# Kernel optimization log

Measured on AMD Instinct MI355X. Metric: run time of the kernel, lower is better.

The kernel has to match this reference:

```python
import jax, jax.numpy as jnp
import numpy as np

HEADS = 4
DIM_HEAD = 32


def setup_inputs() -> dict:
    key = jax.random.key(0)
    k1, k2, k3 = jax.random.split(key, 3)
    B, L, D = 16, 8192, 256
    hidden = HEADS * DIM_HEAD  # 128
    x = jax.random.normal(k1, (B, L, D), dtype=jnp.float32)
    W_qkv = jax.random.normal(k2, (D, 3 * hidden), dtype=jnp.float32) * (D ** -0.5)
    W_out = jax.random.normal(k3, (hidden, D), dtype=jnp.float32) * (hidden ** -0.5)
    b_out = jnp.zeros((D,), dtype=jnp.float32)
    return {"x": x, "W_qkv": W_qkv, "W_out": W_out, "b_out": b_out}


def reference(x, W_qkv, W_out, b_out):
    B, L, D = x.shape
    scale = DIM_HEAD ** -0.5
    # 1x1 conv == per-token matmul
    qkv = jnp.einsum('bld,df->blf', x, W_qkv)  # [B, L, 3*h*dh]
    qkv = qkv.reshape(B, L, 3, HEADS, DIM_HEAD)
    q = jnp.transpose(qkv[:, :, 0], (0, 2, 1, 3)) * scale          # [B, h, L, d]
    k = jax.nn.softmax(jnp.transpose(qkv[:, :, 1], (0, 2, 1, 3)), axis=2)  # softmax over L
    v = jnp.transpose(qkv[:, :, 2], (0, 2, 1, 3))                  # [B, h, L, e]
    context = jnp.einsum('bhld,bhle->bhde', k, v)                  # [B, h, d, e]
    out = jnp.einsum('bhde,bhld->bhle', context, q)                # [B, h, L, e]
    out = jnp.transpose(out, (0, 2, 1, 3)).reshape(B, L, HEADS * DIM_HEAD)
    return jnp.einsum('blf,fd->bld', out, W_out) + b_out
```

## Files before the change

kernel.cpp:

```cpp
#include <hip/hip_runtime.h>
#include <math.h>


#define BL 131072

typedef __attribute__((ext_vector_type(8))) short bf16x8;
typedef __attribute__((ext_vector_type(4))) float f32x4;
typedef __attribute__((ext_vector_type(4))) unsigned u32x4;

__device__ __forceinline__ unsigned cvt_pk2(float a, float b) {
    unsigned r;
    asm("v_cvt_pk_bf16_f32 %0, %1, %2" : "=v"(r) : "v"(a), "v"(b));
    return r;
}
__device__ __forceinline__ ushort bf16_rn(float f) {
    return (ushort)cvt_pk2(f, f);
}
__device__ __forceinline__ float bf16f(ushort h) { return __uint_as_float(((unsigned)h) << 16); }

__device__ __forceinline__ void glds16(const void* g, void* l) {
    __builtin_amdgcn_global_load_lds((const __attribute__((address_space(1))) unsigned int*)g,
                                     (__attribute__((address_space(3))) unsigned int*)l,
                                     16, 0, 0);
}

__global__ __launch_bounds__(256) void prep_kernel(const float* __restrict__ W,
                                                   ushort* __restrict__ wh,
                                                   ushort* __restrict__ wl,
                                                   float* __restrict__ S,
                                                   float* __restrict__ Z) {
    int n = blockIdx.x, k = threadIdx.x;
    float f = W[k * 384 + n];
    ushort h = bf16_rn(f);
    wh[n * 256 + k] = h;
    wl[n * 256 + k] = bf16_rn(f - bf16f(h));
    int i = n * 256 + k;
    if (i < 65536) S[i] = 0.f;
    if (i < 2048) Z[i] = 0.f;
}

__global__ __launch_bounds__(256) void gemm1_kernel(
    const float* __restrict__ X,
    const ushort* __restrict__ Wh, const ushort* __restrict__ Wl,
    ushort* __restrict__ Qh, ushort* __restrict__ Ql,
    float* __restrict__ KV) {
    __shared__ __align__(16) float  As[2][4096];
    __shared__ __align__(16) ushort Bsh[2][4096];
    __shared__ __align__(16) ushort Bsl[2][4096];
    const int tid = threadIdx.x;
    const int wg = blockIdx.x;
    const int xcd = wg & 7;
    const int slot = wg >> 3;
    const int cb = slot % 3;
    const int yb = (slot / 3) * 8 + xcd;
    const int col0 = cb * 128;
    const int row0 = yb * 128;
    const int lane = tid & 63, wave = tid >> 6;
    const int wr = (wave & 1) * 64, wc = (wave >> 1) * 64;
    const int m = lane & 15, quad = lane >> 4;
    const int ra = lane >> 3, pa = lane & 7;
    const int rb = lane >> 2, pb = lane & 3;

    f32x4 acc[4][4] = {};

    auto STAGE = [&](int buf, int k0) {
#pragma unroll
        for (int s = 0; s < 4; ++s) {
            int seg = s * 4 + wave;
            int r = seg * 8 + ra;
            int q = pa ^ (r & 7);
            glds16(&X[(long)(row0 + r) * 256 + k0 + q * 4], &As[buf][seg * 256]);
        }
#pragma unroll
        for (int s = 0; s < 2; ++s) {
            int seg = s * 4 + wave;
            int r = seg * 16 + rb;
            int q = pb ^ ((r >> 1) & 3);
            glds16(&Wh[(long)(col0 + r) * 256 + k0 + q * 8], &Bsh[buf][seg * 512]);
            glds16(&Wl[(long)(col0 + r) * 256 + k0 + q * 8], &Bsl[buf][seg * 512]);
        }
    };

    STAGE(0, 0);
    __syncthreads();

    for (int kt = 0; kt < 8; ++kt) {
        const int cur = kt & 1;
        if (kt < 7) STAGE(cur ^ 1, (kt + 1) * 32);

        bf16x8 bh[4], bl[4];
#pragma unroll
        for (int i = 0; i < 4; ++i) {
            int r = wc + i * 16 + m;
            int p = quad ^ ((r >> 1) & 3);
            bh[i] = *(const bf16x8*)&Bsh[cur][r * 32 + p * 8];
            bl[i] = *(const bf16x8*)&Bsl[cur][r * 32 + p * 8];
        }
#pragma unroll
        for (int i = 0; i < 4; ++i) {
            int r = wr + i * 16 + m;
            int p0 = (quad * 2) ^ (r & 7);
            int p1 = (quad * 2 + 1) ^ (r & 7);
            f32x4 a0 = *(const f32x4*)&As[cur][r * 32 + p0 * 4];
            f32x4 a1 = *(const f32x4*)&As[cur][r * 32 + p1 * 4];
            u32x4 ahw, alw;
#pragma unroll
            for (int e = 0; e < 2; ++e) {
                float f0 = a0[2 * e], f1 = a0[2 * e + 1];
                unsigned h = cvt_pk2(f0, f1);
                ahw[e] = h;
                alw[e] = cvt_pk2(f0 - __uint_as_float(h << 16),
                                 f1 - __uint_as_float(h & 0xFFFF0000u));
            }
#pragma unroll
            for (int e = 0; e < 2; ++e) {
                float f0 = a1[2 * e], f1 = a1[2 * e + 1];
                unsigned h = cvt_pk2(f0, f1);
                ahw[2 + e] = h;
                alw[2 + e] = cvt_pk2(f0 - __uint_as_float(h << 16),
                                     f1 - __uint_as_float(h & 0xFFFF0000u));
            }
            bf16x8 ah = __builtin_bit_cast(bf16x8, ahw);
            bf16x8 al = __builtin_bit_cast(bf16x8, alw);
#pragma unroll
            for (int j = 0; j < 4; ++j) {
                acc[i][j] = __builtin_amdgcn_mfma_f32_16x16x32_bf16(ah, bh[j], acc[i][j], 0, 0, 0);
                acc[i][j] = __builtin_amdgcn_mfma_f32_16x16x32_bf16(ah, bl[j], acc[i][j], 0, 0, 0);
                acc[i][j] = __builtin_amdgcn_mfma_f32_16x16x32_bf16(al, bh[j], acc[i][j], 0, 0, 0);
            }
        }
        __syncthreads();
    }

    if (cb == 0) {
#pragma unroll
        for (int i = 0; i < 4; ++i)
#pragma unroll
            for (int r4 = 0; r4 < 4; ++r4) {
                long row = row0 + wr + i * 16 + quad * 4 + r4;
#pragma unroll
                for (int j = 0; j < 4; ++j) {
                    float v = acc[i][j][r4];
                    int col = wc + j * 16 + m;
                    ushort h = bf16_rn(v);
                    Qh[row * 128 + col] = h;
                    Ql[row * 128 + col] = bf16_rn(v - bf16f(h));
                }
            }
    } else {
        int vofs = (cb == 2) ? 32 : 0;
#pragma unroll
        for (int i = 0; i < 4; ++i)
#pragma unroll
            for (int r4 = 0; r4 < 4; ++r4) {
                long row = row0 + wr + i * 16 + quad * 4 + r4;
                long b = row >> 13, l = row & 8191;
#pragma unroll
                for (int j = 0; j < 4; ++j) {
                    int c = wc + j * 16 + m;
                    int h = c >> 5, dd = c & 31;
                    KV[(((b * 4 + h) * 8192 + l) * 64) + vofs + dd] = acc[i][j][r4];
                }
            }
    }
}

__global__ __launch_bounds__(256) void ksum_hb(const float* __restrict__ KV,
                                               float* __restrict__ S,
                                               float* __restrict__ Z) {
    int bx = blockIdx.x;
    int chunk = bx & 7, bh = bx >> 3;
    const float* slab = KV + ((long)bh * 8192 + chunk * 1024) * 64;
    __shared__ float tile[4128];
    const int tid = threadIdx.x;
    const int w = tid >> 6, lane = tid & 63;
    const int lg = lane >> 3, cc = lane & 7;
    const int combo = w * 8 + cc;
    const int d0 = (combo >> 2) * 4;
    const int e0 = (combo & 3) * 8;
    const int c4 = tid & 15, lrow = tid >> 4;
    float z4[4] = {0.f, 0.f, 0.f, 0.f};
    float acc[4][8] = {};

    for (int t0 = 0; t0 < 1024; t0 += 64) {
#pragma unroll
        for (int u = 0; u < 4; ++u) {
            int l = u * 16 + lrow;
            float4 wv = *(const float4*)&slab[((long)(t0 + l)) * 64 + c4 * 4];
            if (c4 < 8) { wv.x = __expf(wv.x); wv.y = __expf(wv.y); wv.z = __expf(wv.z); wv.w = __expf(wv.w); }
            *(float4*)&tile[l * 64 + (l >> 3) * 4 + c4 * 4] = wv;
        }
        __syncthreads();
#pragma unroll
        for (int j = 0; j < 8; ++j) {
            int l = lg * 8 + j;
            int base = l * 64 + lg * 4;
            f32x4 ev = *(const f32x4*)&tile[base + d0];
            f32x4 v0 = *(const f32x4*)&tile[base + 32 + e0];
            f32x4 v1 = *(const f32x4*)&tile[base + 36 + e0];
#pragma unroll
            for (int q = 0; q < 4; ++q) {
                float e = ev[q];
                z4[q] += e;
                acc[q][0] += e * v0[0]; acc[q][1] += e * v0[1];
                acc[q][2] += e * v0[2]; acc[q][3] += e * v0[3];
                acc[q][4] += e * v1[0]; acc[q][5] += e * v1[1];
                acc[q][6] += e * v1[2]; acc[q][7] += e * v1[3];
            }
        }
        __syncthreads();
    }
#pragma unroll
    for (int q = 0; q < 4; ++q) {
        z4[q] += __shfl_xor(z4[q], 8);
        z4[q] += __shfl_xor(z4[q], 16);
        z4[q] += __shfl_xor(z4[q], 32);
#pragma unroll
        for (int j = 0; j < 8; ++j) {
            acc[q][j] += __shfl_xor(acc[q][j], 8);
            acc[q][j] += __shfl_xor(acc[q][j], 16);
            acc[q][j] += __shfl_xor(acc[q][j], 32);
        }
    }
    if (lg == 0) {
#pragma unroll
        for (int q = 0; q < 4; ++q)
#pragma unroll
            for (int j = 0; j < 8; ++j)
                atomicAdd(&S[((long)bh * 32 + d0 + q) * 32 + e0 + j], acc[q][j]);
        if ((cc & 3) == 0)
#pragma unroll
            for (int q = 0; q < 4; ++q)
                atomicAdd(&Z[bh * 32 + d0 + q], z4[q]);
    }
}

__global__ __launch_bounds__(256) void combine_kernel(const float* __restrict__ S,
                                                      const float* __restrict__ Z,
                                                      const float* __restrict__ Wout,
                                                      ushort* __restrict__ m2h,
                                                      ushort* __restrict__ m2l) {
    int bh = blockIdx.x;
    int b = bh >> 2, h = bh & 3;
    int n = threadIdx.x;
    __shared__ float ctx[32][32];
    __shared__ float zs[32];
    if (n < 32) zs[n] = Z[bh * 32 + n];
    __syncthreads();
#pragma unroll
    for (int t = 0; t < 4; ++t) {
        int idx = t * 256 + n;
        int d = idx >> 5, e = idx & 31;
        ctx[d][e] = S[(long)bh * 1024 + idx] / zs[d];
    }
    __syncthreads();
    const float scale = 0.17677669529663687f;
    float acc[32];
#pragma unroll
    for (int d = 0; d < 32; ++d) acc[d] = 0.f;
    for (int e = 0; e < 32; ++e) {
        float w = Wout[(h * 32 + e) * 256 + n];
#pragma unroll
        for (int d = 0; d < 32; ++d) acc[d] += ctx[d][e] * w;
    }
#pragma unroll
    for (int d = 0; d < 32; ++d) {
        float v = acc[d] * scale;
        long idx = ((long)(b * 256 + n)) * 128 + h * 32 + d;
        ushort hh = bf16_rn(v);
        m2h[idx] = hh;
        m2l[idx] = bf16_rn(v - bf16f(hh));
    }
}

__global__ __launch_bounds__(256) void gemm2_kernel(
    const ushort* __restrict__ Ahp, const ushort* __restrict__ Alp,
    const ushort* __restrict__ Bhp, const ushort* __restrict__ Blp,
    const float* __restrict__ bias, float* __restrict__ out) {
    __shared__ __align__(16) ushort Ash[2][4096];
    __shared__ __align__(16) ushort Asl[2][4096];
    __shared__ __align__(16) ushort Bsh[2][4096];
    __shared__ __align__(16) ushort Bsl[2][4096];
    const int tid = threadIdx.x;
    const int bid = blockIdx.x;
    const int xcd = bid & 7;
    const int u = bid >> 3;
    const int cbl = u & 1;
    const int id = (u >> 1) * 8 + xcd;
    const int col0 = cbl * 128;
    const int row0 = (id & 63) * 128;
    const long bz = id >> 6;
    const ushort* Ah = Ahp + bz * (8192L * 128);
    const ushort* Al = Alp + bz * (8192L * 128);
    const ushort* Bh = Bhp + bz * (256L * 128);
    const ushort* Bl = Blp + bz * (256L * 128);
    const int lane = tid & 63, wave = tid >> 6;
    const int wr = (wave & 1) * 64, wc = (wave >> 1) * 64;
    const int m = lane & 15, quad = lane >> 4;
    const int rb = lane >> 2, pb = lane & 3;

    f32x4 acc[4][4] = {};

    auto STAGE = [&](int buf, int k0) {
#pragma unroll
        for (int s = 0; s < 2; ++s) {
            int seg = s * 4 + wave;
            int r = seg * 16 + rb;
            int q = pb ^ ((r >> 1) & 3);
            glds16(&Ah[(long)(row0 + r) * 128 + k0 + q * 8], &Ash[buf][seg * 512]);
            glds16(&Al[(long)(row0 + r) * 128 + k0 + q * 8], &Asl[buf][seg * 512]);
            glds16(&Bh[(long)(col0 + r) * 128 + k0 + q * 8], &Bsh[buf][seg * 512]);
            glds16(&Bl[(long)(col0 + r) * 128 + k0 + q * 8], &Bsl[buf][seg * 512]);
        }
    };

    STAGE(0, 0);
    __syncthreads();

    for (int kt = 0; kt < 4; ++kt) {
        const int cur = kt & 1;
        if (kt < 3) STAGE(cur ^ 1, (kt + 1) * 32);

        bf16x8 af[2][4], bg[2][4];
#pragma unroll
        for (int i = 0; i < 4; ++i) {
            int rA = wr + i * 16 + m;
            int pA = quad ^ ((rA >> 1) & 3);
            af[0][i] = *(const bf16x8*)&Ash[cur][rA * 32 + pA * 8];
            af[1][i] = *(const bf16x8*)&Asl[cur][rA * 32 + pA * 8];
            int rB = wc + i * 16 + m;
            int pB = quad ^ ((rB >> 1) & 3);
            bg[0][i] = *(const bf16x8*)&Bsh[cur][rB * 32 + pB * 8];
            bg[1][i] = *(const bf16x8*)&Bsl[cur][rB * 32 + pB * 8];
        }
#pragma unroll
        for (int i = 0; i < 4; ++i)
#pragma unroll
            for (int j = 0; j < 4; ++j) {
                acc[i][j] = __builtin_amdgcn_mfma_f32_16x16x32_bf16(af[0][i], bg[0][j], acc[i][j], 0, 0, 0);
                acc[i][j] = __builtin_amdgcn_mfma_f32_16x16x32_bf16(af[0][i], bg[1][j], acc[i][j], 0, 0, 0);
                acc[i][j] = __builtin_amdgcn_mfma_f32_16x16x32_bf16(af[1][i], bg[0][j], acc[i][j], 0, 0, 0);
            }
        __syncthreads();
    }

    float bv[4];
#pragma unroll
    for (int j = 0; j < 4; ++j) bv[j] = bias[col0 + wc + j * 16 + m];
    float* outb = out + bz * (8192L * 256);
#pragma unroll
    for (int i = 0; i < 4; ++i)
#pragma unroll
        for (int r4 = 0; r4 < 4; ++r4) {
            long row = row0 + wr + i * 16 + quad * 4 + r4;
#pragma unroll
            for (int j = 0; j < 4; ++j)
                outb[row * 256 + col0 + wc + j * 16 + m] = acc[i][j][r4] + bv[j];
        }
}

extern "C" void kernel_launch(void* const* d_in, const int* in_sizes, int n_in,
                              void* d_out, int out_size, void* d_ws, size_t ws_size,
                              hipStream_t stream) {
    const float* x     = (const float*)d_in[0];
    const float* W_qkv = (const float*)d_in[1];
    const float* W_out = (const float*)d_in[2];
    const float* b_out = (const float*)d_in[3];
    float* out = (float*)d_out;

    char* p = (char*)d_ws;
    float* kv   = (float*)p;  p += (long)64 * 8192 * 64 * 4;
    float* S    = (float*)p;  p += 65536 * 4;
    float* Z    = (float*)p;  p += 2048 * 4;
    ushort* wth = (ushort*)p; p += 384 * 256 * 2;
    ushort* wtl = (ushort*)p; p += 384 * 256 * 2;
    ushort* qh  = (ushort*)p; p += (long)BL * 128 * 2;
    ushort* ql  = (ushort*)p; p += (long)BL * 128 * 2;
    ushort* m2h = (ushort*)p; p += 16 * 256 * 128 * 2;
    ushort* m2l = (ushort*)p; p += 16 * 256 * 128 * 2;

    prep_kernel<<<384, 256, 0, stream>>>(W_qkv, wth, wtl, S, Z);

    gemm1_kernel<<<3072, 256, 0, stream>>>(x, wth, wtl, qh, ql, kv);

    ksum_hb<<<512, 256, 0, stream>>>(kv, S, Z);
    combine_kernel<<<64, 256, 0, stream>>>(S, Z, W_out, m2h, m2l);

    gemm2_kernel<<<2048, 256, 0, stream>>>(qh, ql, m2h, m2l, b_out, out);
}
```

Before: 429.0 us.

## Pipeline GEMM tiles with two-ahead prefetch, explicit vmcnt waits, and split ksum finer

Both GEMM kernels now issue the first two stages up front and, at each iteration, wait on vmcnt only for the older stage before a raw barrier. The next-but-one stage is issued after the trailing barrier, and MFMA sections run under raised wave priority. This aims to keep global-to-LDS loads in flight across the compute and avoid full drains from __syncthreads. The ksum kernel is split into 32 chunks of 256 rows per head instead of 8 chunks of 1024, launching 2048 blocks for more parallelism. The hand-tuned vmcnt counts must match the number of loads per stage, and more ksum blocks means more partial results to atomically combine.

```diff
diff --git a/kernel.cpp b/kernel.cpp
--- a/kernel.cpp
+++ b/kernel.cpp
@@ -82,12 +82,24 @@
     };
 
     STAGE(0, 0);
-    __syncthreads();
+    STAGE(1, 32);
 
     for (int kt = 0; kt < 8; ++kt) {
         const int cur = kt & 1;
-        if (kt < 7) STAGE(cur ^ 1, (kt + 1) * 32);
-
+        if (kt < 7) asm volatile("s_waitcnt vmcnt(8)" ::: "memory");
+        else        asm volatile("s_waitcnt vmcnt(0)" ::: "memory");
+        __builtin_amdgcn_s_barrier();
+        __builtin_amdgcn_sched_barrier(0);
+
+        f32x4 a0v[4], a1v[4];
+#pragma unroll
+        for (int i = 0; i < 4; ++i) {
+            int r = wr + i * 16 + m;
+            int p0 = (quad * 2) ^ (r & 7);
+            int p1 = (quad * 2 + 1) ^ (r & 7);
+            a0v[i] = *(const f32x4*)&As[cur][r * 32 + p0 * 4];
+            a1v[i] = *(const f32x4*)&As[cur][r * 32 + p1 * 4];
+        }
         bf16x8 bh[4], bl[4];
 #pragma unroll
         for (int i = 0; i < 4; ++i) {
@@ -98,15 +110,10 @@
         }
 #pragma unroll
         for (int i = 0; i < 4; ++i) {
-            int r = wr + i * 16 + m;
-            int p0 = (quad * 2) ^ (r & 7);
-            int p1 = (quad * 2 + 1) ^ (r & 7);
-            f32x4 a0 = *(const f32x4*)&As[cur][r * 32 + p0 * 4];
-            f32x4 a1 = *(const f32x4*)&As[cur][r * 32 + p1 * 4];
             u32x4 ahw, alw;
 #pragma unroll
             for (int e = 0; e < 2; ++e) {
-                float f0 = a0[2 * e], f1 = a0[2 * e + 1];
+                float f0 = a0v[i][2 * e], f1 = a0v[i][2 * e + 1];
                 unsigned h = cvt_pk2(f0, f1);
                 ahw[e] = h;
                 alw[e] = cvt_pk2(f0 - __uint_as_float(h << 16),
@@ -114,7 +121,7 @@
             }
 #pragma unroll
             for (int e = 0; e < 2; ++e) {
-                float f0 = a1[2 * e], f1 = a1[2 * e + 1];
+                float f0 = a1v[i][2 * e], f1 = a1v[i][2 * e + 1];
                 unsigned h = cvt_pk2(f0, f1);
                 ahw[2 + e] = h;
                 alw[2 + e] = cvt_pk2(f0 - __uint_as_float(h << 16),
@@ -122,14 +129,19 @@
             }
             bf16x8 ah = __builtin_bit_cast(bf16x8, ahw);
             bf16x8 al = __builtin_bit_cast(bf16x8, alw);
+            __builtin_amdgcn_s_setprio(1);
 #pragma unroll
             for (int j = 0; j < 4; ++j) {
                 acc[i][j] = __builtin_amdgcn_mfma_f32_16x16x32_bf16(ah, bh[j], acc[i][j], 0, 0, 0);
                 acc[i][j] = __builtin_amdgcn_mfma_f32_16x16x32_bf16(ah, bl[j], acc[i][j], 0, 0, 0);
                 acc[i][j] = __builtin_amdgcn_mfma_f32_16x16x32_bf16(al, bh[j], acc[i][j], 0, 0, 0);
             }
-        }
-        __syncthreads();
+            __builtin_amdgcn_s_setprio(0);
+        }
+        __builtin_amdgcn_sched_barrier(0);
+        __builtin_amdgcn_s_barrier();
+        __builtin_amdgcn_sched_barrier(0);
+        if (kt < 6) STAGE(cur, (kt + 2) * 32);
     }
 
     if (cb == 0) {
@@ -169,8 +181,8 @@
                                                float* __restrict__ S,
                                                float* __restrict__ Z) {
     int bx = blockIdx.x;
-    int chunk = bx & 7, bh = bx >> 3;
-    const float* slab = KV + ((long)bh * 8192 + chunk * 1024) * 64;
+    int chunk = bx & 31, bh = bx >> 5;
+    const float* slab = KV + ((long)bh * 8192 + chunk * 256) * 64;
     __shared__ float tile[4128];
     const int tid = threadIdx.x;
     const int w = tid >> 6, lane = tid & 63;
@@ -182,7 +194,7 @@
     float z4[4] = {0.f, 0.f, 0.f, 0.f};
     float acc[4][8] = {};
 
-    for (int t0 = 0; t0 < 1024; t0 += 64) {
+    for (int t0 = 0; t0 < 256; t0 += 64) {
 #pragma unroll
         for (int u = 0; u < 4; ++u) {
             int l = u * 16 + lrow;
@@ -315,11 +327,14 @@
     };
 
     STAGE(0, 0);
-    __syncthreads();
+    STAGE(1, 32);
 
     for (int kt = 0; kt < 4; ++kt) {
         const int cur = kt & 1;
-        if (kt < 3) STAGE(cur ^ 1, (kt + 1) * 32);
+        if (kt < 3) asm volatile("s_waitcnt vmcnt(8)" ::: "memory");
+        else        asm volatile("s_waitcnt vmcnt(0)" ::: "memory");
+        __builtin_amdgcn_s_barrier();
+        __builtin_amdgcn_sched_barrier(0);
 
         bf16x8 af[2][4], bg[2][4];
 #pragma unroll
@@ -333,6 +348,7 @@
             bg[0][i] = *(const bf16x8*)&Bsh[cur][rB * 32 + pB * 8];
             bg[1][i] = *(const bf16x8*)&Bsl[cur][rB * 32 + pB * 8];
         }
+        __builtin_amdgcn_s_setprio(1);
 #pragma unroll
         for (int i = 0; i < 4; ++i)
 #pragma unroll
@@ -341,7 +357,11 @@
                 acc[i][j] = __builtin_amdgcn_mfma_f32_16x16x32_bf16(af[0][i], bg[1][j], acc[i][j], 0, 0, 0);
                 acc[i][j] = __builtin_amdgcn_mfma_f32_16x16x32_bf16(af[1][i], bg[0][j], acc[i][j], 0, 0, 0);
             }
-        __syncthreads();
+        __builtin_amdgcn_s_setprio(0);
+        __builtin_amdgcn_sched_barrier(0);
+        __builtin_amdgcn_s_barrier();
+        __builtin_amdgcn_sched_barrier(0);
+        if (kt < 2) STAGE(cur, (kt + 2) * 32);
     }
 
     float bv[4];
@@ -383,7 +403,7 @@
 
     gemm1_kernel<<<3072, 256, 0, stream>>>(x, wth, wtl, qh, ql, kv);
 
-    ksum_hb<<<512, 256, 0, stream>>>(kv, S, Z);
+    ksum_hb<<<2048, 256, 0, stream>>>(kv, S, Z);
     combine_kernel<<<64, 256, 0, stream>>>(S, Z, W_out, m2h, m2l);
 
     gemm2_kernel<<<2048, 256, 0, stream>>>(qh, ql, m2h, m2l, b_out, out);
```

Result: slower. 452.9 us (+5.6%).
